# Kernel tuning notes

Hardware: AMD Instinct MI355X
Metric: run time of the kernel (lower is better)

The kernel has to match this reference:

```python
import jax, jax.numpy as jnp
import numpy as np

N_QUBITS = 10
QLCU_LAYERS = 2
FEATURE_DIM = 256
BATCH = 256
N_PARAMS = 5 * N_QUBITS * QLCU_LAYERS  # 100
TWO_PI = 2.0 * np.pi


def _rx_mat(theta):
    # (B,) -> (B,2,2) complex64
    c = jnp.cos(theta / 2).astype(jnp.complex64)
    s = (-1j * jnp.sin(theta / 2)).astype(jnp.complex64)
    return jnp.stack([jnp.stack([c, s], -1), jnp.stack([s, c], -1)], -2)


def _ry_mat(theta):
    c = jnp.cos(theta / 2).astype(jnp.complex64)
    s = jnp.sin(theta / 2).astype(jnp.complex64)
    return jnp.stack([jnp.stack([c, -s], -1), jnp.stack([s, c], -1)], -2)


def _rz_mat(theta):
    e0 = jnp.exp(-0.5j * theta.astype(jnp.complex64))
    e1 = jnp.exp(0.5j * theta.astype(jnp.complex64))
    z = jnp.zeros_like(e0)
    return jnp.stack([jnp.stack([e0, z], -1), jnp.stack([z, e1], -1)], -2)


def _apply_1q(state, U, w):
    # state: (B,)+(2,)*n ; U: (B,2,2) ; wire w (PennyLane wire 0 = most significant)
    s = jnp.moveaxis(state, 1 + w, -1)
    s = jnp.einsum('bij,b...j->b...i', U, s)
    return jnp.moveaxis(s, -1, 1 + w)


def _apply_crx(state, theta, c, t):
    # controlled-RX: apply RX(theta) on target t where control c == 1
    s = jnp.moveaxis(state, (1 + c, 1 + t), (-2, -1))
    U = _rx_mat(theta)
    s1 = jnp.einsum('bij,b...j->b...i', U, s[..., 1, :])
    s = jnp.stack([s[..., 0, :], s1], axis=-2)
    return jnp.moveaxis(s, (-2, -1), (1 + c, 1 + t))


def _circuit(params):
    # params: (B, N_PARAMS) angles. Returns (B, 3*n) expvals [X.., Y.., Z..]
    n = N_QUBITS
    B = params.shape[0]
    state = jnp.zeros((B,) + (2,) * n, jnp.complex64)
    state = state.at[(slice(None),) + (0,) * n].set(1.0)
    idx = 0
    for _ in range(QLCU_LAYERS):
        for i in range(n):
            state = _apply_1q(state, _rx_mat(params[:, idx]), i)
            state = _apply_1q(state, _ry_mat(params[:, idx + 1]), i)
            state = _apply_1q(state, _rz_mat(params[:, idx + 2]), i)
            idx += 3
        for i in range(n):
            state = _apply_crx(state, params[:, idx], i, (i + 1) % n)
            idx += 1
        for i in range(n - 1, -1, -1):
            state = _apply_crx(state, params[:, idx], i, (i - 1) % n)
            idx += 1
    X, Y, Z = [], [], []
    for w in range(n):
        s = jnp.moveaxis(state, 1 + w, -1).reshape(B, -1, 2)
        z01 = jnp.sum(jnp.conj(s[..., 0]) * s[..., 1], axis=1)  # (B,)
        X.append(2.0 * jnp.real(z01))
        Y.append(2.0 * jnp.imag(z01))
        probs = jnp.sum(jnp.abs(s) ** 2, axis=1)  # (B,2)
        Z.append(probs[:, 0] - probs[:, 1])
    return jnp.stack(X + Y + Z, axis=1).astype(jnp.float32)


def _branch(x, W, b, base):
    p = x @ W.T + b            # (B, N_PARAMS)
    p = p + base[None, :]
    p = jax.nn.sigmoid(p) * TWO_PI
    return _circuit(p)


def setup_inputs() -> dict:
    key = jax.random.key(0)
    ks = jax.random.split(key, 16)
    d = {
        'x': jax.random.normal(ks[0], (BATCH, FEATURE_DIM), jnp.float32),
        'W1': jax.random.normal(ks[1], (N_PARAMS, FEATURE_DIM), jnp.float32) * 0.05,
        'b1': jnp.zeros((N_PARAMS,), jnp.float32),
        'W2': jax.random.normal(ks[2], (N_PARAMS, FEATURE_DIM), jnp.float32) * 0.05,
        'b2': jnp.zeros((N_PARAMS,), jnp.float32),
        'W3': jax.random.normal(ks[3], (N_PARAMS, FEATURE_DIM), jnp.float32) * 0.05,
        'b3': jnp.zeros((N_PARAMS,), jnp.float32),
        'base1': jax.random.uniform(ks[4], (N_PARAMS,), jnp.float32) * TWO_PI,
        'base2': jax.random.uniform(ks[5], (N_PARAMS,), jnp.float32) * TWO_PI,
        'base3': jax.random.uniform(ks[6], (N_PARAMS,), jnp.float32) * TWO_PI,
        'alpha_real': jax.random.uniform(ks[7], (1,), jnp.float32),
        'alpha_imag': jnp.zeros((1,), jnp.float32),
        'beta_real': jax.random.uniform(ks[8], (1,), jnp.float32),
        'beta_imag': jnp.zeros((1,), jnp.float32),
        'gamma_real': jax.random.uniform(ks[9], (1,), jnp.float32),
        'gamma_imag': jnp.zeros((1,), jnp.float32),
    }
    return d


def reference(x, W1, b1, W2, b2, W3, b3, base1, base2, base3,
              alpha_real, alpha_imag, beta_real, beta_imag, gamma_real, gamma_imag):
    m1 = _branch(x, W1, b1, base1)  # (B, 3n)
    m2 = _branch(x, W2, b2, base2)
    m3 = _branch(x, W3, b3, base3)
    norm = jnp.sqrt(alpha_real**2 + alpha_imag**2 + beta_real**2 + beta_imag**2
                    + gamma_real**2 + gamma_imag**2 + 1e-9)
    ar, ai = alpha_real / norm, alpha_imag / norm
    br, bi = beta_real / norm, beta_imag / norm
    gr, gi = gamma_real / norm, gamma_imag / norm
    re = ar * m1 + br * m2 + gr * m3
    im = ai * m1 + bi * m2 + gi * m3
    return jnp.sqrt(re * re + im * im)
```

## Files before the change

### kernel.cpp

```cpp
#include <hip/hip_runtime.h>
#include <math.h>

#define NQ 10
#define NPAR 100
#define FDIM 256
#define BATCH 256
#define NOUT 30
#define TWO_PI_F 6.283185307179586f


template<int MASK>
__device__ __forceinline__ float lx(float v) {
    if constexpr (MASK == 1) {
        return __int_as_float(__builtin_amdgcn_update_dpp(
            0, __float_as_int(v), 0xB1, 0xF, 0xF, true));
    } else if constexpr (MASK == 2) {
        return __int_as_float(__builtin_amdgcn_update_dpp(
            0, __float_as_int(v), 0x4E, 0xF, 0xF, true));
    } else if constexpr (MASK == 8) {
        return __int_as_float(__builtin_amdgcn_update_dpp(
            0, __float_as_int(v), 0x128, 0xF, 0xF, true));
    } else if constexpr (MASK == 4) {
        return __int_as_float(__builtin_amdgcn_ds_swizzle(__float_as_int(v), 0x101F));
    } else if constexpr (MASK == 16) {
        return __int_as_float(__builtin_amdgcn_ds_swizzle(__float_as_int(v), 0x401F));
    } else {
        return __shfl_xor(v, 32, 64);
    }
}

template<int MASK>
__device__ __forceinline__ float2 lx2(float2 v) {
    return make_float2(lx<MASK>(v.x), lx<MASK>(v.y));
}

__device__ __forceinline__ float redAll(float v) {
    v += lx<1>(v);  v += lx<2>(v);  v += lx<4>(v);
    v += lx<8>(v);  v += lx<16>(v); v += lx<32>(v);
    return v;
}

__device__ __forceinline__ float2 cmul(float2 a, float2 b) {
    return make_float2(a.x*b.x - a.y*b.y, a.x*b.y + a.y*b.x);
}

template<int BIT>
__device__ __forceinline__ void gate1q(float2 (&st)[16], int lane,
                                       float2 u00, float2 u01, float2 u10, float2 u11)
{
    if constexpr (BIT >= 6) {
        constexpr int rb = 1 << (BIT - 6);
        #pragma unroll
        for (int a = 0; a < 16; ++a) {
            if (a & rb) continue;
            const int a1 = a | rb;
            const float2 A0 = st[a], A1 = st[a1];
            float2 n0, n1;
            n0.x = u00.x*A0.x - u00.y*A0.y + u01.x*A1.x - u01.y*A1.y;
            n0.y = u00.x*A0.y + u00.y*A0.x + u01.x*A1.y + u01.y*A1.x;
            n1.x = u10.x*A0.x - u10.y*A0.y + u11.x*A1.x - u11.y*A1.y;
            n1.y = u10.x*A0.y + u10.y*A0.x + u11.x*A1.y + u11.y*A1.x;
            st[a] = n0; st[a1] = n1;
        }
    } else {
        constexpr int lb = 1 << BIT;
        const bool hi = (lane & lb) != 0;
        const float2 A = hi ? u11 : u00;
        const float2 B = hi ? u10 : u01;
        #pragma unroll
        for (int g = 0; g < 16; g += 4) {
            const float2 p0 = lx2<lb>(st[g+0]);
            const float2 p1 = lx2<lb>(st[g+1]);
            const float2 p2 = lx2<lb>(st[g+2]);
            const float2 p3 = lx2<lb>(st[g+3]);
            const float2 m0 = st[g+0], m1 = st[g+1], m2 = st[g+2], m3 = st[g+3];
            st[g+0] = make_float2(A.x*m0.x - A.y*m0.y + B.x*p0.x - B.y*p0.y,
                                  A.x*m0.y + A.y*m0.x + B.x*p0.y + B.y*p0.x);
            st[g+1] = make_float2(A.x*m1.x - A.y*m1.y + B.x*p1.x - B.y*p1.y,
                                  A.x*m1.y + A.y*m1.x + B.x*p1.y + B.y*p1.x);
            st[g+2] = make_float2(A.x*m2.x - A.y*m2.y + B.x*p2.x - B.y*p2.y,
                                  A.x*m2.y + A.y*m2.x + B.x*p2.y + B.y*p2.x);
            st[g+3] = make_float2(A.x*m3.x - A.y*m3.y + B.x*p3.x - B.y*p3.y,
                                  A.x*m3.y + A.y*m3.x + B.x*p3.y + B.y*p3.x);
        }
    }
}

template<int BC, int BT>
__device__ __forceinline__ void crx(float2 (&st)[16], int lane, float c, float s)
{
    if constexpr (BT >= 6) {
        constexpr int rt = 1 << (BT - 6);
        if constexpr (BC >= 6) {
            constexpr int rc = 1 << (BC - 6);
            #pragma unroll
            for (int a = 0; a < 16; ++a) {
                if (!(a & rc) || (a & rt)) continue;
                const int a1 = a | rt;
                const float2 A0 = st[a], A1 = st[a1];
                float2 n0, n1;
                n0.x = c*A0.x + s*A1.y;  n0.y = c*A0.y - s*A1.x;
                n1.x = c*A1.x + s*A0.y;  n1.y = c*A1.y - s*A0.x;
                st[a] = n0; st[a1] = n1;
            }
        } else {
            constexpr int lc = 1 << BC;
            const bool act = (lane & lc) != 0;
            const float cc = act ? c : 1.f;
            const float ss = act ? s : 0.f;
            #pragma unroll
            for (int a = 0; a < 16; ++a) {
                if (a & rt) continue;
                const int a1 = a | rt;
                const float2 A0 = st[a], A1 = st[a1];
                float2 n0, n1;
                n0.x = cc*A0.x + ss*A1.y;  n0.y = cc*A0.y - ss*A1.x;
                n1.x = cc*A1.x + ss*A0.y;  n1.y = cc*A1.y - ss*A0.x;
                st[a] = n0; st[a1] = n1;
            }
        }
    } else {
        constexpr int lt = 1 << BT;
        if constexpr (BC >= 6) {
            constexpr int rc = 1 << (BC - 6);
            #pragma unroll
            for (int j = 0; j < 8; j += 4) {
                const int a0 = ((j     & ~(rc-1)) << 1) | rc | ((j  ) & (rc-1));
                const int a1 = (((j+1) & ~(rc-1)) << 1) | rc | ((j+1) & (rc-1));
                const int a2 = (((j+2) & ~(rc-1)) << 1) | rc | ((j+2) & (rc-1));
                const int a3 = (((j+3) & ~(rc-1)) << 1) | rc | ((j+3) & (rc-1));
                const float2 p0 = lx2<lt>(st[a0]);
                const float2 p1 = lx2<lt>(st[a1]);
                const float2 p2 = lx2<lt>(st[a2]);
                const float2 p3 = lx2<lt>(st[a3]);
                const float2 m0 = st[a0], m1 = st[a1], m2 = st[a2], m3 = st[a3];
                st[a0] = make_float2(c*m0.x + s*p0.y, c*m0.y - s*p0.x);
                st[a1] = make_float2(c*m1.x + s*p1.y, c*m1.y - s*p1.x);
                st[a2] = make_float2(c*m2.x + s*p2.y, c*m2.y - s*p2.x);
                st[a3] = make_float2(c*m3.x + s*p3.y, c*m3.y - s*p3.x);
            }
        } else {
            constexpr int lc = 1 << BC;
            const bool act = (lane & lc) != 0;
            const float cc = act ? c : 1.f;
            const float ss = act ? s : 0.f;
            #pragma unroll
            for (int g = 0; g < 16; g += 4) {
                const float2 p0 = lx2<lt>(st[g+0]);
                const float2 p1 = lx2<lt>(st[g+1]);
                const float2 p2 = lx2<lt>(st[g+2]);
                const float2 p3 = lx2<lt>(st[g+3]);
                const float2 m0 = st[g+0], m1 = st[g+1], m2 = st[g+2], m3 = st[g+3];
                st[g+0] = make_float2(cc*m0.x + ss*p0.y, cc*m0.y - ss*p0.x);
                st[g+1] = make_float2(cc*m1.x + ss*p1.y, cc*m1.y - ss*p1.x);
                st[g+2] = make_float2(cc*m2.x + ss*p2.y, cc*m2.y - ss*p2.x);
                st[g+3] = make_float2(cc*m3.x + ss*p3.y, cc*m3.y - ss*p3.x);
            }
        }
    }
}

template<int Q>
__device__ __forceinline__ void layer1q(float2 (&st)[16], int lane, const float2* cs, int idx)
{
    if constexpr (Q < NQ) {
        const float2 X = cs[idx], Y = cs[idx + 1], Z = cs[idx + 2];
        const float cx = X.x, sx = X.y, cy = Y.x, sy = Y.y, cz = Z.x, sz = Z.y;
        const float2 m00 = make_float2( cy*cx,  sy*sx);
        const float2 m01 = make_float2(-sy*cx, -cy*sx);
        const float2 m10 = make_float2( sy*cx, -cy*sx);
        const float2 m11 = make_float2( cy*cx, -sy*sx);
        const float2 u00 = make_float2(cz*m00.x + sz*m00.y, cz*m00.y - sz*m00.x);
        const float2 u01 = make_float2(cz*m01.x + sz*m01.y, cz*m01.y - sz*m01.x);
        const float2 u10 = make_float2(cz*m10.x - sz*m10.y, cz*m10.y + sz*m10.x);
        const float2 u11 = make_float2(cz*m11.x - sz*m11.y, cz*m11.y + sz*m11.x);
        gate1q<9 - Q>(st, lane, u00, u01, u10, u11);
        layer1q<Q + 1>(st, lane, cs, idx + 3);
    }
}

template<int Q>
__device__ __forceinline__ void ringF(float2 (&st)[16], int lane, const float2* cs, int idx)
{
    if constexpr (Q < NQ) {
        const float2 p = cs[idx];
        crx<9 - Q, 9 - ((Q + 1) % NQ)>(st, lane, p.x, p.y);
        ringF<Q + 1>(st, lane, cs, idx + 1);
    }
}

template<int Q>
__device__ __forceinline__ void ringB(float2 (&st)[16], int lane, const float2* cs, int idx)
{
    if constexpr (Q >= 0) {
        const float2 p = cs[idx];
        crx<9 - Q, 9 - ((Q + NQ - 1) % NQ)>(st, lane, p.x, p.y);
        ringB<Q - 1>(st, lane, cs, idx + 1);
    }
}

__device__ __forceinline__ void col0(const float2* cs, int w, float2& u00, float2& u10)
{
    const float2 X = cs[3*w], Y = cs[3*w + 1], Z = cs[3*w + 2];
    const float cx = X.x, sx = X.y, cy = Y.x, sy = Y.y, cz = Z.x, sz = Z.y;
    const float2 m00 = make_float2(cy*cx,  sy*sx);
    const float2 m10 = make_float2(sy*cx, -cy*sx);
    u00 = make_float2(cz*m00.x + sz*m00.y, cz*m00.y - sz*m00.x);
    u10 = make_float2(cz*m10.x - sz*m10.y, cz*m10.y + sz*m10.x);
}

template<int W>
__device__ __forceinline__ void measureAll(const float2 (&st)[16], int lane, float* m_row)
{
    if constexpr (W < NQ) {
        constexpr int B = 9 - W;
        float sre = 0.f, smm = 0.f, szz = 0.f;
        if constexpr (B >= 6) {
            constexpr int rb = 1 << (B - 6);
            #pragma unroll
            for (int a = 0; a < 16; ++a) {
                if (a & rb) continue;
                const int a1 = a | rb;
                const float2 A0 = st[a], A1 = st[a1];
                sre += A0.x*A1.x + A0.y*A1.y;
                smm += A0.x*A1.y - A0.y*A1.x;
                szz += A0.x*A0.x + A0.y*A0.y - A1.x*A1.x - A1.y*A1.y;
            }
            sre *= 2.f; smm *= 2.f;
        } else {
            constexpr int lb = 1 << B;
            const float sgn = (lane & lb) ? -1.f : 1.f;
            #pragma unroll
            for (int g = 0; g < 16; g += 4) {
                const float2 p0 = lx2<lb>(st[g+0]);
                const float2 p1 = lx2<lb>(st[g+1]);
                const float2 p2 = lx2<lb>(st[g+2]);
                const float2 p3 = lx2<lb>(st[g+3]);
                const float2 m0 = st[g+0], m1 = st[g+1], m2 = st[g+2], m3 = st[g+3];
                sre += m0.x*p0.x + m0.y*p0.y + m1.x*p1.x + m1.y*p1.y
                     + m2.x*p2.x + m2.y*p2.y + m3.x*p3.x + m3.y*p3.y;
                smm += sgn * ((m0.x*p0.y - m0.y*p0.x) + (m1.x*p1.y - m1.y*p1.x)
                            + (m2.x*p2.y - m2.y*p2.x) + (m3.x*p3.y - m3.y*p3.x));
                szz += sgn * ((m0.x*m0.x + m0.y*m0.y - p0.x*p0.x - p0.y*p0.y)
                            + (m1.x*m1.x + m1.y*m1.y - p1.x*p1.x - p1.y*p1.y)
                            + (m2.x*m2.x + m2.y*m2.y - p2.x*p2.x - p2.y*p2.y)
                            + (m3.x*m3.x + m3.y*m3.y - p3.x*p3.x - p3.y*p3.y));
            }
            szz *= 0.5f;
        }
        sre = redAll(sre);
        smm = redAll(smm);
        szz = redAll(szz);
        if (lane == 0) {
            m_row[W]      = sre;
            m_row[10 + W] = smm;
            m_row[20 + W] = szz;
        }
        measureAll<W + 1>(st, lane, m_row);
    }
}

__global__ __launch_bounds__(192) void qsb_fused(
    const float* __restrict__ x,
    const float* __restrict__ W1, const float* __restrict__ b1, const float* __restrict__ base1,
    const float* __restrict__ W2, const float* __restrict__ b2, const float* __restrict__ base2,
    const float* __restrict__ W3, const float* __restrict__ b3, const float* __restrict__ base3,
    const float* __restrict__ ar_, const float* __restrict__ ai_,
    const float* __restrict__ br_, const float* __restrict__ bi_,
    const float* __restrict__ gr_, const float* __restrict__ gi_,
    float* __restrict__ out)
{
    const int b    = blockIdx.x;
    const int wv   = threadIdx.x >> 6;
    const int lane = threadIdx.x & 63;

    const float* W    = (wv == 0) ? W1    : (wv == 1) ? W2    : W3;
    const float* bias = (wv == 0) ? b1    : (wv == 1) ? b2    : b3;
    const float* base = (wv == 0) ? base1 : (wv == 1) ? base2 : base3;

    __shared__ float2 css[3][NPAR];
    __shared__ float  mloc[3][NOUT];
    float2* cs = css[wv];

    if (lane < 50) {
        const int p0 = 2 * lane;
        const float4* xr = reinterpret_cast<const float4*>(x + (size_t)b * FDIM);
        const float4* w0 = reinterpret_cast<const float4*>(W + (size_t)p0 * FDIM);
        const float4* w1 = reinterpret_cast<const float4*>(W + (size_t)(p0 + 1) * FDIM);
        float acc0 = 0.f, acc1 = 0.f;
        #pragma unroll 8
        for (int k = 0; k < FDIM / 4; ++k) {
            const float4 xv = xr[k];
            const float4 a  = w0[k];
            const float4 bb = w1[k];
            acc0 += xv.x*a.x  + xv.y*a.y  + xv.z*a.z  + xv.w*a.w;
            acc1 += xv.x*bb.x + xv.y*bb.y + xv.z*bb.z + xv.w*bb.w;
        }
        acc0 += bias[p0]     + base[p0];
        acc1 += bias[p0 + 1] + base[p0 + 1];
        const float t0 = TWO_PI_F / (1.f + __expf(-acc0));
        const float t1 = TWO_PI_F / (1.f + __expf(-acc1));
        float s0, c0, s1, c1;
        __sincosf(0.5f * t0, &s0, &c0);
        __sincosf(0.5f * t1, &s1, &c1);
        cs[p0]     = make_float2(c0, s0);
        cs[p0 + 1] = make_float2(c1, s1);
    }
    __syncthreads();

    float2 st[16];
    {
        float2 lp = make_float2(1.f, 0.f);
        #pragma unroll
        for (int bb = 0; bb < 6; ++bb) {
            float2 u00, u10;
            col0(cs, 9 - bb, u00, u10);
            const float2 sel = ((lane >> bb) & 1) ? u10 : u00;
            lp = cmul(lp, sel);
        }
        float2 v3[2], v2[2], v1[2], v0[2];
        col0(cs, 3, v3[0], v3[1]);
        col0(cs, 2, v2[0], v2[1]);
        col0(cs, 1, v1[0], v1[1]);
        col0(cs, 0, v0[0], v0[1]);
        #pragma unroll
        for (int a = 0; a < 16; ++a) {
            float2 t = cmul(v3[a & 1], v2[(a >> 1) & 1]);
            t = cmul(t, cmul(v1[(a >> 2) & 1], v0[(a >> 3) & 1]));
            st[a] = cmul(t, lp);
        }
    }

    ringF<0>(st, lane, cs, 30);
    ringB<NQ - 1>(st, lane, cs, 40);
    layer1q<0>(st, lane, cs, 50);
    ringF<0>(st, lane, cs, 80);
    ringB<NQ - 1>(st, lane, cs, 90);

    measureAll<0>(st, lane, mloc[wv]);
    __syncthreads();

    if (threadIdx.x < NOUT) {
        const int i = threadIdx.x;
        const float ar = ar_[0], ai = ai_[0];
        const float br = br_[0], bi = bi_[0];
        const float gr = gr_[0], gi = gi_[0];
        const float inv = 1.f / sqrtf(ar*ar + ai*ai + br*br + bi*bi
                                      + gr*gr + gi*gi + 1e-9f);
        const float m1 = mloc[0][i], m2 = mloc[1][i], m3 = mloc[2][i];
        const float re = (ar * m1 + br * m2 + gr * m3) * inv;
        const float im = (ai * m1 + bi * m2 + gi * m3) * inv;
        out[(size_t)b * NOUT + i] = sqrtf(re * re + im * im);
    }
}

extern "C" void kernel_launch(void* const* d_in, const int* in_sizes, int n_in,
                              void* d_out, int out_size, void* d_ws, size_t ws_size,
                              hipStream_t stream)
{
    (void)in_sizes; (void)n_in; (void)out_size; (void)d_ws; (void)ws_size;
    const float* x     = (const float*)d_in[0];
    const float* W1    = (const float*)d_in[1];
    const float* b1    = (const float*)d_in[2];
    const float* W2    = (const float*)d_in[3];
    const float* b2    = (const float*)d_in[4];
    const float* W3    = (const float*)d_in[5];
    const float* b3    = (const float*)d_in[6];
    const float* base1 = (const float*)d_in[7];
    const float* base2 = (const float*)d_in[8];
    const float* base3 = (const float*)d_in[9];
    const float* ar    = (const float*)d_in[10];
    const float* ai    = (const float*)d_in[11];
    const float* br    = (const float*)d_in[12];
    const float* bi    = (const float*)d_in[13];
    const float* gr    = (const float*)d_in[14];
    const float* gi    = (const float*)d_in[15];

    qsb_fused<<<dim3(BATCH), dim3(192), 0, stream>>>(
        x, W1, b1, base1, W2, b2, base2, W3, b3, base3,
        ar, ai, br, bi, gr, gi, (float*)d_out);
}
```

Measured before the change: 111.0 us.

## Split each wavefront into two half-waves simulating two batch items

Each 64-lane wave now holds two independent 10-qubit statevectors, one per 32-lane half. Each lane keeps 32 amplitudes in registers instead of 16, and one fewer qubit is mapped across lanes. The grid shrinks to half the batch, lane-exchange gates drop the cross-32 shuffle, and reductions lose a step. In exchange register pressure doubles, which may lower occupancy or cause spills, and the angle matvec is restructured so each lane computes up to four params.

```diff
diff --git a/kernel.cpp b/kernel.cpp
--- a/kernel.cpp
+++ b/kernel.cpp
@@ -7,6 +7,7 @@
 #define BATCH 256
 #define NOUT 30
 #define TWO_PI_F 6.283185307179586f
+#define LB 5
 
 
 template<int MASK>
@@ -22,10 +23,8 @@
             0, __float_as_int(v), 0x128, 0xF, 0xF, true));
     } else if constexpr (MASK == 4) {
         return __int_as_float(__builtin_amdgcn_ds_swizzle(__float_as_int(v), 0x101F));
-    } else if constexpr (MASK == 16) {
+    } else {
         return __int_as_float(__builtin_amdgcn_ds_swizzle(__float_as_int(v), 0x401F));
-    } else {
-        return __shfl_xor(v, 32, 64);
     }
 }
 
@@ -36,7 +35,7 @@
 
 __device__ __forceinline__ float redAll(float v) {
     v += lx<1>(v);  v += lx<2>(v);  v += lx<4>(v);
-    v += lx<8>(v);  v += lx<16>(v); v += lx<32>(v);
+    v += lx<8>(v);  v += lx<16>(v);
     return v;
 }
 
@@ -45,13 +44,13 @@
 }
 
 template<int BIT>
-__device__ __forceinline__ void gate1q(float2 (&st)[16], int lane,
+__device__ __forceinline__ void gate1q(float2 (&st)[32], int slane,
                                        float2 u00, float2 u01, float2 u10, float2 u11)
 {
-    if constexpr (BIT >= 6) {
-        constexpr int rb = 1 << (BIT - 6);
-        #pragma unroll
-        for (int a = 0; a < 16; ++a) {
+    if constexpr (BIT >= LB) {
+        constexpr int rb = 1 << (BIT - LB);
+        #pragma unroll
+        for (int a = 0; a < 32; ++a) {
             if (a & rb) continue;
             const int a1 = a | rb;
             const float2 A0 = st[a], A1 = st[a1];
@@ -64,11 +63,11 @@
         }
     } else {
         constexpr int lb = 1 << BIT;
-        const bool hi = (lane & lb) != 0;
+        const bool hi = (slane & lb) != 0;
         const float2 A = hi ? u11 : u00;
         const float2 B = hi ? u10 : u01;
         #pragma unroll
-        for (int g = 0; g < 16; g += 4) {
+        for (int g = 0; g < 32; g += 4) {
             const float2 p0 = lx2<lb>(st[g+0]);
             const float2 p1 = lx2<lb>(st[g+1]);
             const float2 p2 = lx2<lb>(st[g+2]);
@@ -87,14 +86,14 @@
 }
 
 template<int BC, int BT>
-__device__ __forceinline__ void crx(float2 (&st)[16], int lane, float c, float s)
-{
-    if constexpr (BT >= 6) {
-        constexpr int rt = 1 << (BT - 6);
-        if constexpr (BC >= 6) {
-            constexpr int rc = 1 << (BC - 6);
-            #pragma unroll
-            for (int a = 0; a < 16; ++a) {
+__device__ __forceinline__ void crx(float2 (&st)[32], int slane, float c, float s)
+{
+    if constexpr (BT >= LB) {
+        constexpr int rt = 1 << (BT - LB);
+        if constexpr (BC >= LB) {
+            constexpr int rc = 1 << (BC - LB);
+            #pragma unroll
+            for (int a = 0; a < 32; ++a) {
                 if (!(a & rc) || (a & rt)) continue;
                 const int a1 = a | rt;
                 const float2 A0 = st[a], A1 = st[a1];
@@ -105,11 +104,11 @@
             }
         } else {
             constexpr int lc = 1 << BC;
-            const bool act = (lane & lc) != 0;
+            const bool act = (slane & lc) != 0;
             const float cc = act ? c : 1.f;
             const float ss = act ? s : 0.f;
             #pragma unroll
-            for (int a = 0; a < 16; ++a) {
+            for (int a = 0; a < 32; ++a) {
                 if (a & rt) continue;
                 const int a1 = a | rt;
                 const float2 A0 = st[a], A1 = st[a1];
@@ -121,10 +120,10 @@
         }
     } else {
         constexpr int lt = 1 << BT;
-        if constexpr (BC >= 6) {
-            constexpr int rc = 1 << (BC - 6);
-            #pragma unroll
-            for (int j = 0; j < 8; j += 4) {
+        if constexpr (BC >= LB) {
+            constexpr int rc = 1 << (BC - LB);
+            #pragma unroll
+            for (int j = 0; j < 16; j += 4) {
                 const int a0 = ((j     & ~(rc-1)) << 1) | rc | ((j  ) & (rc-1));
                 const int a1 = (((j+1) & ~(rc-1)) << 1) | rc | ((j+1) & (rc-1));
                 const int a2 = (((j+2) & ~(rc-1)) << 1) | rc | ((j+2) & (rc-1));
@@ -141,11 +140,11 @@
             }
         } else {
             constexpr int lc = 1 << BC;
-            const bool act = (lane & lc) != 0;
+            const bool act = (slane & lc) != 0;
             const float cc = act ? c : 1.f;
             const float ss = act ? s : 0.f;
             #pragma unroll
-            for (int g = 0; g < 16; g += 4) {
+            for (int g = 0; g < 32; g += 4) {
                 const float2 p0 = lx2<lt>(st[g+0]);
                 const float2 p1 = lx2<lt>(st[g+1]);
                 const float2 p2 = lx2<lt>(st[g+2]);
@@ -161,7 +160,7 @@
 }
 
 template<int Q>
-__device__ __forceinline__ void layer1q(float2 (&st)[16], int lane, const float2* cs, int idx)
+__device__ __forceinline__ void layer1q(float2 (&st)[32], int slane, const float2* cs, int idx)
 {
     if constexpr (Q < NQ) {
         const float2 X = cs[idx], Y = cs[idx + 1], Z = cs[idx + 2];
@@ -174,28 +173,28 @@
         const float2 u01 = make_float2(cz*m01.x + sz*m01.y, cz*m01.y - sz*m01.x);
         const float2 u10 = make_float2(cz*m10.x - sz*m10.y, cz*m10.y + sz*m10.x);
         const float2 u11 = make_float2(cz*m11.x - sz*m11.y, cz*m11.y + sz*m11.x);
-        gate1q<9 - Q>(st, lane, u00, u01, u10, u11);
-        layer1q<Q + 1>(st, lane, cs, idx + 3);
+        gate1q<9 - Q>(st, slane, u00, u01, u10, u11);
+        layer1q<Q + 1>(st, slane, cs, idx + 3);
     }
 }
 
 template<int Q>
-__device__ __forceinline__ void ringF(float2 (&st)[16], int lane, const float2* cs, int idx)
+__device__ __forceinline__ void ringF(float2 (&st)[32], int slane, const float2* cs, int idx)
 {
     if constexpr (Q < NQ) {
         const float2 p = cs[idx];
-        crx<9 - Q, 9 - ((Q + 1) % NQ)>(st, lane, p.x, p.y);
-        ringF<Q + 1>(st, lane, cs, idx + 1);
+        crx<9 - Q, 9 - ((Q + 1) % NQ)>(st, slane, p.x, p.y);
+        ringF<Q + 1>(st, slane, cs, idx + 1);
     }
 }
 
 template<int Q>
-__device__ __forceinline__ void ringB(float2 (&st)[16], int lane, const float2* cs, int idx)
+__device__ __forceinline__ void ringB(float2 (&st)[32], int slane, const float2* cs, int idx)
 {
     if constexpr (Q >= 0) {
         const float2 p = cs[idx];
-        crx<9 - Q, 9 - ((Q + NQ - 1) % NQ)>(st, lane, p.x, p.y);
-        ringB<Q - 1>(st, lane, cs, idx + 1);
+        crx<9 - Q, 9 - ((Q + NQ - 1) % NQ)>(st, slane, p.x, p.y);
+        ringB<Q - 1>(st, slane, cs, idx + 1);
     }
 }
 
@@ -210,15 +209,15 @@
 }
 
 template<int W>
-__device__ __forceinline__ void measureAll(const float2 (&st)[16], int lane, float* m_row)
+__device__ __forceinline__ void measureAll(const float2 (&st)[32], int slane, float* m_row)
 {
     if constexpr (W < NQ) {
         constexpr int B = 9 - W;
         float sre = 0.f, smm = 0.f, szz = 0.f;
-        if constexpr (B >= 6) {
-            constexpr int rb = 1 << (B - 6);
-            #pragma unroll
-            for (int a = 0; a < 16; ++a) {
+        if constexpr (B >= LB) {
+            constexpr int rb = 1 << (B - LB);
+            #pragma unroll
+            for (int a = 0; a < 32; ++a) {
                 if (a & rb) continue;
                 const int a1 = a | rb;
                 const float2 A0 = st[a], A1 = st[a1];
@@ -229,9 +228,9 @@
             sre *= 2.f; smm *= 2.f;
         } else {
             constexpr int lb = 1 << B;
-            const float sgn = (lane & lb) ? -1.f : 1.f;
-            #pragma unroll
-            for (int g = 0; g < 16; g += 4) {
+            const float sgn = (slane & lb) ? -1.f : 1.f;
+            #pragma unroll
+            for (int g = 0; g < 32; g += 4) {
                 const float2 p0 = lx2<lb>(st[g+0]);
                 const float2 p1 = lx2<lb>(st[g+1]);
                 const float2 p2 = lx2<lb>(st[g+2]);
@@ -251,12 +250,12 @@
         sre = redAll(sre);
         smm = redAll(smm);
         szz = redAll(szz);
-        if (lane == 0) {
+        if (slane == 0) {
             m_row[W]      = sre;
             m_row[10 + W] = smm;
             m_row[20 + W] = szz;
         }
-        measureAll<W + 1>(st, lane, m_row);
+        measureAll<W + 1>(st, slane, m_row);
     }
 }
 
@@ -270,87 +269,87 @@
     const float* __restrict__ gr_, const float* __restrict__ gi_,
     float* __restrict__ out)
 {
-    const int b    = blockIdx.x;
-    const int wv   = threadIdx.x >> 6;
-    const int lane = threadIdx.x & 63;
-
-    const float* W    = (wv == 0) ? W1    : (wv == 1) ? W2    : W3;
+    const int bp    = blockIdx.x;
+    const int wv    = threadIdx.x >> 6;
+    const int lane  = threadIdx.x & 63;
+    const int slane = lane & 31;
+    const int half  = lane >> 5;
+    const int bi    = 2 * bp + half;
+
+    const float* Wp   = (wv == 0) ? W1    : (wv == 1) ? W2    : W3;
     const float* bias = (wv == 0) ? b1    : (wv == 1) ? b2    : b3;
     const float* base = (wv == 0) ? base1 : (wv == 1) ? base2 : base3;
 
-    __shared__ float2 css[3][NPAR];
-    __shared__ float  mloc[3][NOUT];
-    float2* cs = css[wv];
-
-    if (lane < 50) {
-        const int p0 = 2 * lane;
-        const float4* xr = reinterpret_cast<const float4*>(x + (size_t)b * FDIM);
-        const float4* w0 = reinterpret_cast<const float4*>(W + (size_t)p0 * FDIM);
-        const float4* w1 = reinterpret_cast<const float4*>(W + (size_t)(p0 + 1) * FDIM);
-        float acc0 = 0.f, acc1 = 0.f;
-        #pragma unroll 8
-        for (int k = 0; k < FDIM / 4; ++k) {
-            const float4 xv = xr[k];
-            const float4 a  = w0[k];
-            const float4 bb = w1[k];
-            acc0 += xv.x*a.x  + xv.y*a.y  + xv.z*a.z  + xv.w*a.w;
-            acc1 += xv.x*bb.x + xv.y*bb.y + xv.z*bb.z + xv.w*bb.w;
-        }
-        acc0 += bias[p0]     + base[p0];
-        acc1 += bias[p0 + 1] + base[p0 + 1];
-        const float t0 = TWO_PI_F / (1.f + __expf(-acc0));
-        const float t1 = TWO_PI_F / (1.f + __expf(-acc1));
-        float s0, c0, s1, c1;
-        __sincosf(0.5f * t0, &s0, &c0);
-        __sincosf(0.5f * t1, &s1, &c1);
-        cs[p0]     = make_float2(c0, s0);
-        cs[p0 + 1] = make_float2(c1, s1);
+    __shared__ float2 css[3][2][NPAR];
+    __shared__ float  mloc[3][2][NOUT];
+    float2* cs = css[wv][half];
+
+    const float4* xr = reinterpret_cast<const float4*>(x + (size_t)bi * FDIM);
+    #pragma unroll
+    for (int it = 0; it < 4; ++it) {
+        const int p = slane + 32 * it;
+        if (p < NPAR) {
+            const float4* wr = reinterpret_cast<const float4*>(Wp + (size_t)p * FDIM);
+            float acc = 0.f;
+            #pragma unroll 8
+            for (int k = 0; k < FDIM / 4; ++k) {
+                const float4 xv = xr[k];
+                const float4 wv4 = wr[k];
+                acc += xv.x*wv4.x + xv.y*wv4.y + xv.z*wv4.z + xv.w*wv4.w;
+            }
+            acc += bias[p] + base[p];
+            const float t = TWO_PI_F / (1.f + __expf(-acc));
+            float sn, cn;
+            __sincosf(0.5f * t, &sn, &cn);
+            cs[p] = make_float2(cn, sn);
+        }
     }
     __syncthreads();
 
-    float2 st[16];
+    float2 st[32];
     {
         float2 lp = make_float2(1.f, 0.f);
         #pragma unroll
-        for (int bb = 0; bb < 6; ++bb) {
+        for (int bb = 0; bb < LB; ++bb) {
             float2 u00, u10;
             col0(cs, 9 - bb, u00, u10);
-            const float2 sel = ((lane >> bb) & 1) ? u10 : u00;
+            const float2 sel = ((slane >> bb) & 1) ? u10 : u00;
             lp = cmul(lp, sel);
         }
-        float2 v3[2], v2[2], v1[2], v0[2];
-        col0(cs, 3, v3[0], v3[1]);
-        col0(cs, 2, v2[0], v2[1]);
-        col0(cs, 1, v1[0], v1[1]);
-        col0(cs, 0, v0[0], v0[1]);
-        #pragma unroll
-        for (int a = 0; a < 16; ++a) {
-            float2 t = cmul(v3[a & 1], v2[(a >> 1) & 1]);
-            t = cmul(t, cmul(v1[(a >> 2) & 1], v0[(a >> 3) & 1]));
+        float2 vr[5][2];
+        #pragma unroll
+        for (int j = 0; j < 5; ++j) col0(cs, 4 - j, vr[j][0], vr[j][1]);
+        #pragma unroll
+        for (int a = 0; a < 32; ++a) {
+            float2 t = cmul(vr[0][a & 1], vr[1][(a >> 1) & 1]);
+            const float2 u = cmul(vr[2][(a >> 2) & 1], vr[3][(a >> 3) & 1]);
+            t = cmul(t, u);
+            t = cmul(t, vr[4][(a >> 4) & 1]);
             st[a] = cmul(t, lp);
         }
     }
 
-    ringF<0>(st, lane, cs, 30);
-    ringB<NQ - 1>(st, lane, cs, 40);
-    layer1q<0>(st, lane, cs, 50);
-    ringF<0>(st, lane, cs, 80);
-    ringB<NQ - 1>(st, lane, cs, 90);
-
-    measureAll<0>(st, lane, mloc[wv]);
+    ringF<0>(st, slane, cs, 30);
+    ringB<NQ - 1>(st, slane, cs, 40);
+    layer1q<0>(st, slane, cs, 50);
+    ringF<0>(st, slane, cs, 80);
+    ringB<NQ - 1>(st, slane, cs, 90);
+
+    measureAll<0>(st, slane, mloc[wv][half]);
     __syncthreads();
 
-    if (threadIdx.x < NOUT) {
-        const int i = threadIdx.x;
+    if (threadIdx.x < 2 * NOUT) {
+        const int item = threadIdx.x / NOUT;
+        const int j    = threadIdx.x % NOUT;
         const float ar = ar_[0], ai = ai_[0];
-        const float br = br_[0], bi = bi_[0];
+        const float br = br_[0], bi2 = bi_[0];
         const float gr = gr_[0], gi = gi_[0];
-        const float inv = 1.f / sqrtf(ar*ar + ai*ai + br*br + bi*bi
+        const float inv = 1.f / sqrtf(ar*ar + ai*ai + br*br + bi2*bi2
                                       + gr*gr + gi*gi + 1e-9f);
-        const float m1 = mloc[0][i], m2 = mloc[1][i], m3 = mloc[2][i];
+        const float m1 = mloc[0][item][j], m2 = mloc[1][item][j], m3 = mloc[2][item][j];
         const float re = (ar * m1 + br * m2 + gr * m3) * inv;
-        const float im = (ai * m1 + bi * m2 + gi * m3) * inv;
-        out[(size_t)b * NOUT + i] = sqrtf(re * re + im * im);
+        const float im = (ai * m1 + bi2 * m2 + gi * m3) * inv;
+        out[(size_t)(2 * bp + item) * NOUT + j] = sqrtf(re * re + im * im);
     }
 }
 
@@ -376,7 +375,7 @@
     const float* gr    = (const float*)d_in[14];
     const float* gi    = (const float*)d_in[15];
 
-    qsb_fused<<<dim3(BATCH), dim3(192), 0, stream>>>(
+    qsb_fused<<<dim3(BATCH / 2), dim3(192), 0, stream>>>(
         x, W1, b1, base1, W2, b2, base2, W3, b3, base3,
         ar, ai, br, bi, gr, gi, (float*)d_out);
 }
```

Result: slower. 130.7 us (+17.8%).
